# Optimization experiments

Measured on AMD Instinct MI355X. Metric: run time of the kernel, lower is better.

## Reference

```python
import jax, jax.numpy as jnp
import numpy as np

N = 50000      # nodes
E = 800000     # edges (before self-loops)
F_IN = 256     # nfeat
HEADS = 8      # nhead
C1 = 16        # hidden_sizes (per-head channels of conv1)
NCLS = 40      # nclass
NEG_SLOPE = 0.2


def setup_inputs() -> dict:
    key = jax.random.key(0)
    ks = jax.random.split(key, 12)
    s = 0.1
    x = jax.random.normal(ks[0], (N, F_IN), dtype=jnp.float32)
    edge_index = jax.random.randint(ks[1], (2, E), 0, N, dtype=jnp.int64)
    edge_attr = jax.random.normal(ks[2], (E,), dtype=jnp.float32)  # unused by forward
    W1 = jax.random.normal(ks[3], (F_IN, HEADS * C1), dtype=jnp.float32) * s
    att_src1 = jax.random.normal(ks[4], (HEADS, C1), dtype=jnp.float32) * s
    att_dst1 = jax.random.normal(ks[5], (HEADS, C1), dtype=jnp.float32) * s
    b1 = jnp.zeros((HEADS * C1,), dtype=jnp.float32)
    W2 = jax.random.normal(ks[6], (HEADS * C1, NCLS), dtype=jnp.float32) * s
    att_src2 = jax.random.normal(ks[7], (1, NCLS), dtype=jnp.float32) * s
    att_dst2 = jax.random.normal(ks[8], (1, NCLS), dtype=jnp.float32) * s
    b2 = jnp.zeros((NCLS,), dtype=jnp.float32)
    return {"x": x, "edge_index": edge_index, "edge_attr": edge_attr,
            "W1": W1, "att_src1": att_src1, "att_dst1": att_dst1, "b1": b1,
            "W2": W2, "att_src2": att_src2, "att_dst2": att_dst2, "b2": b2}


def gat_layer(x, W, att_src, att_dst, bias, src, dst, concat):
    """PyG-style GATConv (eval mode, no dropout). src/dst include self-loops."""
    H, C = att_src.shape
    h = (x @ W).reshape(-1, H, C)                     # [N,H,C]
    a_src = (h * att_src[None]).sum(-1)               # [N,H]
    a_dst = (h * att_dst[None]).sum(-1)               # [N,H]
    e = jax.nn.leaky_relu(a_src[src] + a_dst[dst], NEG_SLOPE)  # [Etot,H]
    # segment softmax over destination neighborhoods
    m = jax.ops.segment_max(e, dst, num_segments=N)   # [N,H]
    m = jax.lax.stop_gradient(jnp.where(jnp.isfinite(m), m, 0.0))
    p = jnp.exp(e - m[dst])
    denom = jax.ops.segment_sum(p, dst, num_segments=N)
    alpha = p / (denom[dst] + 1e-16)                  # [Etot,H]
    out = jax.ops.segment_sum(alpha[:, :, None] * h[src], dst, num_segments=N)  # [N,H,C]
    out = out.reshape(-1, H * C) if concat else out.mean(axis=1)
    return out + bias


def reference(x, edge_index, edge_attr, W1, att_src1, att_dst1, b1, W2, att_src2, att_dst2, b2):
    # add self loops (PyG GATConv default)
    loops = jnp.arange(N, dtype=edge_index.dtype)
    src = jnp.concatenate([edge_index[0], loops])
    dst = jnp.concatenate([edge_index[1], loops])
    # eval mode: F.dropout is identity
    h = jax.nn.elu(gat_layer(x, W1, att_src1, att_dst1, b1, src, dst, concat=True))
    final = gat_layer(h, W2, att_src2, att_dst2, b2, src, dst, concat=False)
    return final, jax.nn.log_softmax(final, axis=1)
```

## Files before the change

kernel.cpp:

```cpp
#include <hip/hip_runtime.h>

#define NN 50000
#define EE 800000
#define FIN 256
#define HD 8
#define C1 16
#define HC 128
#define NC 40
#define NEG 0.2f
#define CAP 64
#define R2 32
#define BM 64
#define NB_P 98
#define GB1 (NB_P * 8)
#define NP_N (NN / 8)

typedef __attribute__((ext_vector_type(8))) short short8;
typedef __attribute__((ext_vector_type(4))) float f32x4;
union FragU { uint4 u; short8 s; };

__device__ __forceinline__ float leaky(float v){ return v > 0.f ? v : NEG * v; }

__device__ __forceinline__ unsigned int f2bf(float f){
  unsigned int u = __float_as_uint(f);
  u += 0x7fffu + ((u >> 16) & 1u);
  return u >> 16;
}
__device__ __forceinline__ unsigned int pack2bf(float a, float b){
  return f2bf(a) | (f2bf(b) << 16);
}
__device__ __forceinline__ float bflo(unsigned int u){ return __uint_as_float(u << 16); }
__device__ __forceinline__ float bfhi(unsigned int u){ return __uint_as_float(u & 0xffff0000u); }

__global__ __launch_bounds__(256) void k_prep(const float* __restrict__ W1,
                                              uint4* __restrict__ W1bfs){
  int f = blockIdx.x * 256 + threadIdx.x;
  int lane = f & 63, nt = (f >> 6) & 7, kt = f >> 9;
  int quad = lane >> 4, l16 = lane & 15;
  const float* src = W1 + (size_t)(kt * 32 + quad * 8) * HC + nt * 16 + l16;
  unsigned int p[4];
#pragma unroll
  for (int jj = 0; jj < 4; jj++){
    float v0 = src[(size_t)(2 * jj) * HC];
    float v1 = src[(size_t)(2 * jj + 1) * HC];
    p[jj] = pack2bf(v0, v1);
  }
  W1bfs[f] = make_uint4(p[0], p[1], p[2], p[3]);
}

__global__ __launch_bounds__(256) void k_gemm1(const float* __restrict__ x,
                                               const uint4* __restrict__ W1bfs,
                                               const float* __restrict__ att_s,
                                               const float* __restrict__ att_d,
                                               const int* __restrict__ ei,
                                               unsigned short* __restrict__ h1b,
                                               float* __restrict__ as1,
                                               float* __restrict__ ad1,
                                               int* __restrict__ cnt,
                                               int* __restrict__ srcp){
  const int tid = threadIdx.x;
  const int part = blockIdx.x & 7, rank = blockIdx.x >> 3;
  const int lo = part * NP_N, hi = lo + NP_N;
  for (int e = rank * 256 + tid; e < EE; e += NB_P * 256){
    int d = ei[EE + e];
    if (d >= lo && d < hi){
      int s = ei[e];
      int pos = atomicAdd(&cnt[d], 1);
      if (pos < CAP) srcp[d * CAP + pos] = s;
    }
  }

  const int wave = tid >> 6, lane = tid & 63;
  const int quad = lane >> 4, l16 = lane & 15;
  const int m0 = blockIdx.x * BM + wave * 16;
  int arow = m0 + l16; if (arow >= NN) arow = NN - 1;
  const float* xr = x + (size_t)arow * FIN;

  f32x4 acc[8];
#pragma unroll
  for (int t = 0; t < 8; t++) acc[t] = (f32x4){0.f, 0.f, 0.f, 0.f};

#pragma unroll
  for (int kt = 0; kt < 8; kt++){
    const float4 a0 = *(const float4*)(xr + kt * 32 + quad * 8);
    const float4 a1 = *(const float4*)(xr + kt * 32 + quad * 8 + 4);
    FragU af;
    af.u = make_uint4(pack2bf(a0.x, a0.y), pack2bf(a0.z, a0.w),
                      pack2bf(a1.x, a1.y), pack2bf(a1.z, a1.w));
    FragU bf[8];
#pragma unroll
    for (int nt = 0; nt < 8; nt++)
      bf[nt].u = W1bfs[(kt * 8 + nt) * 64 + lane];
#pragma unroll
    for (int nt = 0; nt < 8; nt++)
      acc[nt] = __builtin_amdgcn_mfma_f32_16x16x32_bf16(af.s, bf[nt].s, acc[nt], 0, 0, 0);
  }

  float sv[8], dv[8];
#pragma unroll
  for (int h = 0; h < 8; h++){ sv[h] = att_s[h * 16 + l16]; dv[h] = att_d[h * 16 + l16]; }
#pragma unroll
  for (int r = 0; r < 4; r++){
    const int gr = m0 + quad * 4 + r;
    float s[8], d[8];
#pragma unroll
    for (int h = 0; h < 8; h++){ s[h] = acc[h][r] * sv[h]; d[h] = acc[h][r] * dv[h]; }
#pragma unroll
    for (int o = 1; o < 16; o <<= 1){
#pragma unroll
      for (int h = 0; h < 8; h++){ s[h] += __shfl_xor(s[h], o); d[h] += __shfl_xor(d[h], o); }
    }
    if (gr < NN){
#pragma unroll
      for (int h = 0; h < 8; h++)
        h1b[(size_t)gr * HC + h * 16 + l16] = (unsigned short)f2bf(acc[h][r]);
      if (l16 == 0){
        *(float4*)(as1 + gr * 8)     = make_float4(s[0], s[1], s[2], s[3]);
        *(float4*)(as1 + gr * 8 + 4) = make_float4(s[4], s[5], s[6], s[7]);
        *(float4*)(ad1 + gr * 8)     = make_float4(d[0], d[1], d[2], d[3]);
        *(float4*)(ad1 + gr * 8 + 4) = make_float4(d[4], d[5], d[6], d[7]);
      }
    }
  }
}

__global__ __launch_bounds__(64) void k_agg1(const int* __restrict__ srcp,
                                             const int* __restrict__ cnt,
                                             const float* __restrict__ as1,
                                             const float* __restrict__ ad1,
                                             const unsigned short* __restrict__ h1b,
                                             const float* __restrict__ b1,
                                             unsigned short* __restrict__ h2b){
  const int n = blockIdx.x, lane = threadIdx.x;
  const int q = lane >> 4, t = lane & 15, h = t >> 1;
  const int base = n * CAP;
  int deg = cnt[n]; if (deg > CAP) deg = CAP;
  const float adg = ad1[n * 8 + h];
  float m = -3.0e38f, den = 0.f;
  float acc[8];
#pragma unroll
  for (int c = 0; c < 8; c++) acc[c] = 0.f;

  if (q == 0){
    const uint4 hv = *(const uint4*)(h1b + (size_t)n * HC + t * 8);
    m = leaky(as1[n * 8 + h] + adg);
    den = 1.f;
    acc[0] = bflo(hv.x); acc[1] = bfhi(hv.x);
    acc[2] = bflo(hv.y); acc[3] = bfhi(hv.y);
    acc[4] = bflo(hv.z); acc[5] = bfhi(hv.z);
    acc[6] = bflo(hv.w); acc[7] = bfhi(hv.w);
  }

  int i = q;
  int sA = (i < deg) ? srcp[base + i] : n;
  uint4 hA = *(const uint4*)(h1b + (size_t)sA * HC + t * 8);
  float aA = as1[sA * 8 + h];
  int sB = (i + 4 < deg) ? srcp[base + i + 4] : n;
  while (i < deg){
    const uint4 hB = *(const uint4*)(h1b + (size_t)sB * HC + t * 8);
    const float aB = as1[sB * 8 + h];
    const int sC = (i + 8 < deg) ? srcp[base + i + 8] : n;
    float v = leaky(aA + adg);
    float mn = fmaxf(m, v);
    float r = __expf(m - mn), w = __expf(v - mn);
    den = den * r + w;
    acc[0] = acc[0] * r + w * bflo(hA.x); acc[1] = acc[1] * r + w * bfhi(hA.x);
    acc[2] = acc[2] * r + w * bflo(hA.y); acc[3] = acc[3] * r + w * bfhi(hA.y);
    acc[4] = acc[4] * r + w * bflo(hA.z); acc[5] = acc[5] * r + w * bfhi(hA.z);
    acc[6] = acc[6] * r + w * bflo(hA.w); acc[7] = acc[7] * r + w * bfhi(hA.w);
    m = mn;
    hA = hB; aA = aB; sA = sB; sB = sC;
    i += 4;
  }
#pragma unroll
  for (int o = 16; o <= 32; o <<= 1){
    float mo = __shfl_xor(m, o);
    float dno = __shfl_xor(den, o);
    float mn = fmaxf(m, mo);
    float ra = __expf(m - mn), rb = __expf(mo - mn);
    den = den * ra + dno * rb;
#pragma unroll
    for (int c = 0; c < 8; c++){
      float ao = __shfl_xor(acc[c], o);
      acc[c] = acc[c] * ra + ao * rb;
    }
    m = mn;
  }
  if (q == 0){
    float invd = 1.f / (den + 1e-16f);
    float o8[8];
    const float4 bA = *(const float4*)(b1 + t * 8);
    const float4 bB = *(const float4*)(b1 + t * 8 + 4);
    o8[0] = acc[0] * invd + bA.x; o8[1] = acc[1] * invd + bA.y;
    o8[2] = acc[2] * invd + bA.z; o8[3] = acc[3] * invd + bA.w;
    o8[4] = acc[4] * invd + bB.x; o8[5] = acc[5] * invd + bB.y;
    o8[6] = acc[6] * invd + bB.z; o8[7] = acc[7] * invd + bB.w;
#pragma unroll
    for (int c = 0; c < 8; c++) o8[c] = (o8[c] > 0.f) ? o8[c] : (__expf(o8[c]) - 1.f);
    uint4 pk;
    pk.x = pack2bf(o8[0], o8[1]); pk.y = pack2bf(o8[2], o8[3]);
    pk.z = pack2bf(o8[4], o8[5]); pk.w = pack2bf(o8[6], o8[7]);
    *(uint4*)(h2b + (size_t)n * HC + t * 8) = pk;
  }
}

__global__ __launch_bounds__(256) void k_gemm2(const unsigned short* __restrict__ h2b,
                                               const float* __restrict__ W2,
                                               const float* __restrict__ att_s2,
                                               const float* __restrict__ att_d2,
                                               unsigned short* __restrict__ gb,
                                               float* __restrict__ as2,
                                               float* __restrict__ ad2){
  __shared__ float hs[R2][HC + 2];
  __shared__ float w2s[HC * NC];
  const int tid = threadIdx.x;
  const int r0 = blockIdx.x * R2;
  for (int i = tid; i < HC * NC; i += 256) w2s[i] = W2[i];
  for (int i = tid; i < R2 * (HC / 2); i += 256){
    int r = i / (HC / 2), c = i % (HC / 2);
    unsigned int u = (r0 + r < NN) ? ((const unsigned int*)h2b)[(size_t)(r0 + r) * (HC / 2) + c] : 0u;
    hs[r][2 * c]     = bflo(u);
    hs[r][2 * c + 1] = bfhi(u);
  }
  __syncthreads();
  const int r = tid >> 3, j = tid & 7;
  float acc[5] = {0.f, 0.f, 0.f, 0.f, 0.f};
  for (int k = 0; k < HC; k++){
    float hv = hs[r][k];
#pragma unroll
    for (int q = 0; q < 5; q++) acc[q] += hv * w2s[k * NC + j + 8 * q];
  }
  const int node = r0 + r;
  if (node < NN){
    float s = 0.f, d = 0.f;
#pragma unroll
    for (int q = 0; q < 5; q++){
      int c = j + 8 * q;
      gb[(size_t)node * NC + c] = (unsigned short)f2bf(acc[q]);
      s += acc[q] * att_s2[c];
      d += acc[q] * att_d2[c];
    }
#pragma unroll
    for (int o = 1; o < 8; o <<= 1){ s += __shfl_xor(s, o); d += __shfl_xor(d, o); }
    if (j == 0){ as2[node] = s; ad2[node] = d; }
  }
}

__global__ __launch_bounds__(64) void k_agg2(const int* __restrict__ srcp,
                                             const int* __restrict__ cnt,
                                             const float* __restrict__ as2,
                                             const float* __restrict__ ad2,
                                             const unsigned short* __restrict__ gb,
                                             const float* __restrict__ b2,
                                             float* __restrict__ out){
  const int n = blockIdx.x, lane = threadIdx.x;
  const int half = lane >> 5, c2 = lane & 31;
  const int base = n * CAP;
  int deg = cnt[n]; if (deg > CAP) deg = CAP;
  const float ad = ad2[n];
  const bool act = (c2 < 20);
  float m = -3.0e38f, den = 0.f, ax = 0.f, ay = 0.f;
  if (half == 0){
    m = leaky(as2[n] + ad);
    den = 1.f;
    if (act){
      unsigned int u = *(const unsigned int*)(gb + (size_t)n * NC + c2 * 2);
      ax = bflo(u); ay = bfhi(u);
    }
  }
  int i = half;
  int sA = (i < deg) ? srcp[base + i] : n;
  while (i < deg){
    int sB = (i + 2 < deg) ? srcp[base + i + 2] : n;
    float v = leaky(as2[sA] + ad);
    float gx = 0.f, gy = 0.f;
    if (act){
      unsigned int u = *(const unsigned int*)(gb + (size_t)sA * NC + c2 * 2);
      gx = bflo(u); gy = bfhi(u);
    }
    float mn = fmaxf(m, v);
    float r = __expf(m - mn), w = __expf(v - mn);
    den = den * r + w;
    ax = ax * r + w * gx; ay = ay * r + w * gy;
    m = mn;
    sA = sB; i += 2;
  }
  float mo = __shfl_xor(m, 32), dno = __shfl_xor(den, 32);
  float bx = __shfl_xor(ax, 32), by = __shfl_xor(ay, 32);
  float mn = fmaxf(m, mo);
  float ra = __expf(m - mn), rb = __expf(mo - mn);
  den = den * ra + dno * rb;
  ax = ax * ra + bx * rb; ay = ay * ra + by * rb;
  __shared__ float fin[NC];
  if (half == 0 && act){
    float invd = 1.f / (den + 1e-16f);
    float f0 = ax * invd + b2[c2 * 2];
    float f1 = ay * invd + b2[c2 * 2 + 1];
    out[(size_t)n * NC + c2 * 2]     = f0;
    out[(size_t)n * NC + c2 * 2 + 1] = f1;
    fin[c2 * 2] = f0; fin[c2 * 2 + 1] = f1;
  }
  __syncthreads();
  float v = (lane < NC) ? fin[lane] : -3.4e38f;
  float mx = v;
#pragma unroll
  for (int o = 32; o; o >>= 1) mx = fmaxf(mx, __shfl_xor(mx, o));
  float ex = (lane < NC) ? __expf(v - mx) : 0.f;
#pragma unroll
  for (int o = 32; o; o >>= 1) ex += __shfl_xor(ex, o);
  float lse = mx + __logf(ex);
  if (lane < NC) out[(size_t)(NN * NC) + (size_t)n * NC + lane] = v - lse;
}

extern "C" void kernel_launch(void* const* d_in, const int* in_sizes, int n_in,
                              void* d_out, int out_size, void* d_ws, size_t ws_size,
                              hipStream_t stream){
  const float* x      = (const float*)d_in[0];
  const int*   ei     = (const int*)  d_in[1];
  const float* W1     = (const float*)d_in[3];
  const float* att_s1 = (const float*)d_in[4];
  const float* att_d1 = (const float*)d_in[5];
  const float* b1     = (const float*)d_in[6];
  const float* W2     = (const float*)d_in[7];
  const float* att_s2 = (const float*)d_in[8];
  const float* att_d2 = (const float*)d_in[9];
  const float* b2     = (const float*)d_in[10];
  float* out = (float*)d_out;

  char* wp = (char*)d_ws;
  uint4* W1bfs = (uint4*)wp;                 wp += (size_t)4096 * 16;
  unsigned short* h1b = (unsigned short*)wp; wp += (size_t)NN * HC * 2;
  unsigned short* h2b = (unsigned short*)wp; wp += (size_t)NN * HC * 2;
  unsigned short* gb  = (unsigned short*)wp; wp += (size_t)NN * NC * 2;
  float* as1 = (float*)wp;                   wp += (size_t)NN * HD * 4;
  float* ad1 = (float*)wp;                   wp += (size_t)NN * HD * 4;
  float* as2 = (float*)wp;                   wp += (size_t)NN * 4;
  float* ad2 = (float*)wp;                   wp += (size_t)NN * 4;
  int* cnt   = (int*)wp;                     wp += (size_t)NN * 4;
  int* srcp  = (int*)wp;                     wp += (size_t)NN * CAP * 4;

  hipMemsetAsync(cnt, 0, (size_t)NN * sizeof(int), stream);
  k_prep  <<<16, 256, 0, stream>>>(W1, W1bfs);
  k_gemm1 <<<GB1, 256, 0, stream>>>(x, W1bfs, att_s1, att_d1, ei, h1b, as1, ad1, cnt, srcp);
  k_agg1  <<<NN, 64, 0, stream>>>(srcp, cnt, as1, ad1, h1b, b1, h2b);
  k_gemm2 <<<(NN + R2 - 1) / R2, 256, 0, stream>>>(h2b, W2, att_s2, att_d2, gb, as2, ad2);
  k_agg2  <<<NN, 64, 0, stream>>>(srcp, cnt, as2, ad2, gb, b2, out);
}
```

Measured before the change: 284.3 us.

## Split GEMM1 K across waves with LDS reduction; pack 4 nodes per agg block

The first GEMM now uses 32-row tiles and twice as many blocks. Each pair of waves splits the K dimension in half and combines partial accumulators through shared memory. This gives more parallelism for the edge bucketing loop and the MFMA work. The aggregation kernels now process four nodes per 256-thread block instead of one node per 64-thread block, which cuts the number of blocks and the per-block launch overhead. Risks include the added LDS traffic and syncthreads in GEMM1, and idle waves after the early return.

```diff
diff --git a/kernel.cpp b/kernel.cpp
--- a/kernel.cpp
+++ b/kernel.cpp
@@ -10,8 +10,8 @@
 #define NEG 0.2f
 #define CAP 64
 #define R2 32
-#define BM 64
-#define NB_P 98
+#define BM 32
+#define NB_P 196
 #define GB1 (NB_P * 8)
 #define NP_N (NN / 8)
 
@@ -58,6 +58,7 @@
                                                float* __restrict__ ad1,
                                                int* __restrict__ cnt,
                                                int* __restrict__ srcp){
+  __shared__ float cmb[2][32][64];
   const int tid = threadIdx.x;
   const int part = blockIdx.x & 7, rank = blockIdx.x >> 3;
   const int lo = part * NP_N, hi = lo + NP_N;
@@ -71,8 +72,9 @@
   }
 
   const int wave = tid >> 6, lane = tid & 63;
+  const int tile = wave & 1, khalf = wave >> 1;
   const int quad = lane >> 4, l16 = lane & 15;
-  const int m0 = blockIdx.x * BM + wave * 16;
+  const int m0 = blockIdx.x * BM + tile * 16;
   int arow = m0 + l16; if (arow >= NN) arow = NN - 1;
   const float* xr = x + (size_t)arow * FIN;
 
@@ -81,7 +83,8 @@
   for (int t = 0; t < 8; t++) acc[t] = (f32x4){0.f, 0.f, 0.f, 0.f};
 
 #pragma unroll
-  for (int kt = 0; kt < 8; kt++){
+  for (int kk = 0; kk < 4; kk++){
+    const int kt = khalf * 4 + kk;
     const float4 a0 = *(const float4*)(xr + kt * 32 + quad * 8);
     const float4 a1 = *(const float4*)(xr + kt * 32 + quad * 8 + 4);
     FragU af;
@@ -94,6 +97,23 @@
 #pragma unroll
     for (int nt = 0; nt < 8; nt++)
       acc[nt] = __builtin_amdgcn_mfma_f32_16x16x32_bf16(af.s, bf[nt].s, acc[nt], 0, 0, 0);
+  }
+
+  if (khalf){
+    float* p = &cmb[tile][0][lane];
+#pragma unroll
+    for (int nt = 0; nt < 8; nt++)
+#pragma unroll
+      for (int r = 0; r < 4; r++) p[(nt * 4 + r) * 64] = acc[nt][r];
+  }
+  __syncthreads();
+  if (khalf) return;
+  {
+    const float* p = &cmb[tile][0][lane];
+#pragma unroll
+    for (int nt = 0; nt < 8; nt++)
+#pragma unroll
+      for (int r = 0; r < 4; r++) acc[nt][r] += p[(nt * 4 + r) * 64];
   }
 
   float sv[8], dv[8];
@@ -124,14 +144,15 @@
   }
 }
 
-__global__ __launch_bounds__(64) void k_agg1(const int* __restrict__ srcp,
-                                             const int* __restrict__ cnt,
-                                             const float* __restrict__ as1,
-                                             const float* __restrict__ ad1,
-                                             const unsigned short* __restrict__ h1b,
-                                             const float* __restrict__ b1,
-                                             unsigned short* __restrict__ h2b){
-  const int n = blockIdx.x, lane = threadIdx.x;
+__global__ __launch_bounds__(256) void k_agg1(const int* __restrict__ srcp,
+                                              const int* __restrict__ cnt,
+                                              const float* __restrict__ as1,
+                                              const float* __restrict__ ad1,
+                                              const unsigned short* __restrict__ h1b,
+                                              const float* __restrict__ b1,
+                                              unsigned short* __restrict__ h2b){
+  const int lane = threadIdx.x & 63;
+  const int n = blockIdx.x * 4 + (threadIdx.x >> 6);
   const int q = lane >> 4, t = lane & 15, h = t >> 1;
   const int base = n * CAP;
   int deg = cnt[n]; if (deg > CAP) deg = CAP;
@@ -246,14 +267,15 @@
   }
 }
 
-__global__ __launch_bounds__(64) void k_agg2(const int* __restrict__ srcp,
-                                             const int* __restrict__ cnt,
-                                             const float* __restrict__ as2,
-                                             const float* __restrict__ ad2,
-                                             const unsigned short* __restrict__ gb,
-                                             const float* __restrict__ b2,
-                                             float* __restrict__ out){
-  const int n = blockIdx.x, lane = threadIdx.x;
+__global__ __launch_bounds__(256) void k_agg2(const int* __restrict__ srcp,
+                                              const int* __restrict__ cnt,
+                                              const float* __restrict__ as2,
+                                              const float* __restrict__ ad2,
+                                              const unsigned short* __restrict__ gb,
+                                              const float* __restrict__ b2,
+                                              float* __restrict__ out){
+  const int lane = threadIdx.x & 63, w = threadIdx.x >> 6;
+  const int n = blockIdx.x * 4 + w;
   const int half = lane >> 5, c2 = lane & 31;
   const int base = n * CAP;
   int deg = cnt[n]; if (deg > CAP) deg = CAP;
@@ -279,9 +301,9 @@
       gx = bflo(u); gy = bfhi(u);
     }
     float mn = fmaxf(m, v);
-    float r = __expf(m - mn), w = __expf(v - mn);
-    den = den * r + w;
-    ax = ax * r + w * gx; ay = ay * r + w * gy;
+    float r = __expf(m - mn), wgt = __expf(v - mn);
+    den = den * r + wgt;
+    ax = ax * r + wgt * gx; ay = ay * r + wgt * gy;
     m = mn;
     sA = sB; i += 2;
   }
@@ -291,17 +313,17 @@
   float ra = __expf(m - mn), rb = __expf(mo - mn);
   den = den * ra + dno * rb;
   ax = ax * ra + bx * rb; ay = ay * ra + by * rb;
-  __shared__ float fin[NC];
+  __shared__ float fin[4][NC];
   if (half == 0 && act){
     float invd = 1.f / (den + 1e-16f);
     float f0 = ax * invd + b2[c2 * 2];
     float f1 = ay * invd + b2[c2 * 2 + 1];
     out[(size_t)n * NC + c2 * 2]     = f0;
     out[(size_t)n * NC + c2 * 2 + 1] = f1;
-    fin[c2 * 2] = f0; fin[c2 * 2 + 1] = f1;
+    fin[w][c2 * 2] = f0; fin[w][c2 * 2 + 1] = f1;
   }
   __syncthreads();
-  float v = (lane < NC) ? fin[lane] : -3.4e38f;
+  float v = (lane < NC) ? fin[w][lane] : -3.4e38f;
   float mx = v;
 #pragma unroll
   for (int o = 32; o; o >>= 1) mx = fmaxf(mx, __shfl_xor(mx, o));
@@ -342,7 +364,7 @@
   hipMemsetAsync(cnt, 0, (size_t)NN * sizeof(int), stream);
   k_prep  <<<16, 256, 0, stream>>>(W1, W1bfs);
   k_gemm1 <<<GB1, 256, 0, stream>>>(x, W1bfs, att_s1, att_d1, ei, h1b, as1, ad1, cnt, srcp);
-  k_agg1  <<<NN, 64, 0, stream>>>(srcp, cnt, as1, ad1, h1b, b1, h2b);
+  k_agg1  <<<NN / 4, 256, 0, stream>>>(srcp, cnt, as1, ad1, h1b, b1, h2b);
   k_gemm2 <<<(NN + R2 - 1) / R2, 256, 0, stream>>>(h2b, W2, att_s2, att_d2, gb, as2, ad2);
-  k_agg2  <<<NN, 64, 0, stream>>>(srcp, cnt, as2, ad2, gb, b2, out);
-}
+  k_agg2  <<<NN / 4, 256, 0, stream>>>(srcp, cnt, as2, ad2, gb, b2, out);
+}
```

New measurement: 303.6 us. +6.8%, slower.
